# Optimization experiments

Hardware: AMD Instinct MI355X
Metric: run time of the kernel (lower is better)

Reference implementation:

```python
import jax, jax.numpy as jnp
import numpy as np
import math

NUM_HEADS = 8
EPS = 1e-5
LEAKY_SLOPE = 0.01


def _attention(q, k, v, mask):
    # q:[S,64] k,v:[T,64] -> [S,64]; scale by sqrt(d) per source (q.shape[1])
    s = (q @ k.T) / math.sqrt(q.shape[1])
    if mask:
        S, T = s.shape
        tri = jnp.tril(jnp.ones((S, T), dtype=bool))
        s = jnp.where(tri, s, -jnp.inf)
    return jax.nn.softmax(s, axis=1) @ v


def _mha(q, k, v, w_o, mask):
    # all heads share the same (q,k,v) in the source, so cat over heads == tile
    head = _attention(q, k, v, mask)            # [S,64]
    concat = jnp.tile(head, (1, NUM_HEADS))     # [S,512]
    return concat @ w_o


def _layernorm(x, g, b):
    mu = jnp.mean(x, axis=-1, keepdims=True)
    var = jnp.var(x, axis=-1, keepdims=True)
    return (x - mu) * jax.lax.rsqrt(var + EPS) * g + b


def setup_inputs() -> dict:
    key = jax.random.key(0)
    ks = jax.random.split(key, 12)
    S, D, P, H = 8192, 512, 64, 2048
    sd = 1.0 / math.sqrt(D)
    return {
        "encoder_output": jax.random.normal(ks[0], (S, D), jnp.float32),
        "previous_stage_output": jax.random.normal(ks[1], (S, D), jnp.float32),
        "wq_m": jax.random.normal(ks[2], (D, P), jnp.float32) * sd,
        "wk_m": jax.random.normal(ks[3], (D, P), jnp.float32) * sd,
        "wv_m": jax.random.normal(ks[4], (D, P), jnp.float32) * sd,
        "wq_c": jax.random.normal(ks[5], (D, P), jnp.float32) * sd,
        "wk_c": jax.random.normal(ks[6], (D, P), jnp.float32) * sd,
        "wv_c": jax.random.normal(ks[7], (D, P), jnp.float32) * sd,
        "w_o": jax.random.normal(ks[8], (D, D), jnp.float32) * sd,
        "ln_g": jnp.ones((D,), jnp.float32),
        "ln_b": jnp.zeros((D,), jnp.float32),
        "w1": jax.random.normal(ks[9], (D, H), jnp.float32) * sd,
        "b1": jnp.zeros((H,), jnp.float32),
        "w2": jax.random.normal(ks[10], (H, D), jnp.float32) * (1.0 / math.sqrt(H)),
        "b2": jnp.zeros((D,), jnp.float32),
    }


def reference(encoder_output, previous_stage_output, wq_m, wk_m, wv_m,
              wq_c, wk_c, wv_c, w_o, ln_g, ln_b, w1, b1, w2, b2):
    prev = previous_stage_output
    # masked (causal) self-attention over previous decoder output
    masked_mh = _mha(prev @ wq_m, prev @ wk_m, prev @ wv_m, w_o, mask=True)
    # cross attention: q from masked output, k/v from encoder output
    mh = _mha(masked_mh @ wq_c, encoder_output @ wk_c, encoder_output @ wv_c,
              w_o, mask=False)
    x = _layernorm(mh + prev, ln_g, ln_b)
    h = x @ w1 + b1
    h = jnp.where(h >= 0, h, LEAKY_SLOPE * h)
    ffn = h @ w2 + b2
    out = _layernorm(ffn + x, ln_g, ln_b)
    return (encoder_output, out)
```

## Files before the change

kernel.cpp:

```cpp
#include <hip/hip_runtime.h>
#include <hip/hip_bf16.h>

typedef unsigned short u16;
typedef __attribute__((ext_vector_type(4))) float f32x4;
typedef __attribute__((ext_vector_type(8))) __bf16 bf16x8;
typedef __attribute__((ext_vector_type(8))) short short8;
typedef __attribute__((ext_vector_type(4))) short s16x4;

constexpr int SEQ = 8192;
constexpr int DM  = 512;
constexpr int HD  = 64;
constexpr int HFF = 2048;

__device__ __forceinline__ float b2f(u16 u){
  union { unsigned int i; float f; } v; v.i = ((unsigned int)u) << 16; return v.f;
}
__device__ __forceinline__ u16 f2b(float f){
  union { float f; unsigned int i; } v; v.f = f;
  unsigned int r = v.i + 0x7FFFu + ((v.i >> 16) & 1u);
  return (u16)(r >> 16);
}

__device__ __forceinline__ void gload16(const u16* g, u16* lds){
  __builtin_amdgcn_global_load_lds(
      (const __attribute__((address_space(1))) void*)g,
      (__attribute__((address_space(3))) void*)lds, 16, 0, 0);
}

__global__ __launch_bounds__(256) void copycvt_k(const float* __restrict__ in,
                                                 float* __restrict__ outf,
                                                 u16* __restrict__ outb, long n8){
  long i = blockIdx.x * 256L + threadIdx.x;
  if(i >= n8) return;
  f32x4 a = ((const f32x4*)in)[i*2];
  f32x4 b = ((const f32x4*)in)[i*2+1];
  ((f32x4*)outf)[i*2]   = a;
  ((f32x4*)outf)[i*2+1] = b;
  u16 ov[8];
  for(int j=0;j<4;j++){ ov[j] = f2b(a[j]); ov[4+j] = f2b(b[j]); }
  ((short8*)outb)[i] = *(short8*)ov;
}

__global__ __launch_bounds__(256) void cvt_k(const float* __restrict__ in,
                                             u16* __restrict__ out, long n8){
  long i = blockIdx.x * 256L + threadIdx.x;
  if(i >= n8) return;
  f32x4 a = ((const f32x4*)in)[i*2];
  f32x4 b = ((const f32x4*)in)[i*2+1];
  u16 ov[8];
  for(int j=0;j<4;j++){ ov[j] = f2b(a[j]); ov[4+j] = f2b(b[j]); }
  ((short8*)out)[i] = *(short8*)ov;
}

__global__ __launch_bounds__(256) void wtrans6_k(const float* __restrict__ w0,
                                                 const float* __restrict__ w1,
                                                 const float* __restrict__ w2,
                                                 const float* __restrict__ w3,
                                                 const float* __restrict__ w4,
                                                 const float* __restrict__ w5,
                                                 u16* __restrict__ out){
  __shared__ u16 t[32][33];
  const float* ins[6] = {w0,w1,w2,w3,w4,w5};
  const float* in = ins[blockIdx.z];
  u16* o = out + (long)blockIdx.z * 32768;
  int c0 = blockIdx.x*32, r0 = blockIdx.y*32;
  int tx = threadIdx.x, ty = threadIdx.y;
  for(int i=0;i<4;i++)
    t[ty+i*8][tx] = f2b(in[(long)(r0+ty+i*8)*HD + c0+tx]);
  __syncthreads();
  for(int i=0;i<4;i++) o[(long)(c0+ty+i*8)*DM + r0+tx] = t[tx][ty+i*8];
}

template<int IN_F>
__global__ __launch_bounds__(256) void transpose_k(const void* __restrict__ inp,
                                                   u16* __restrict__ out, int R, int C){
  __shared__ u16 t[32][33];
  int c0 = blockIdx.x*32, r0 = blockIdx.y*32;
  int tx = threadIdx.x, ty = threadIdx.y;
  for(int i=0;i<4;i++){
    long idx = (long)(r0+ty+i*8)*C + c0+tx;
    u16 v;
    if constexpr (IN_F) v = f2b(((const float*)inp)[idx]);
    else                v = ((const u16*)inp)[idx];
    t[ty+i*8][tx] = v;
  }
  __syncthreads();
  for(int i=0;i<4;i++) out[(long)(c0+ty+i*8)*R + r0+tx] = t[tx][ty+i*8];
}

__global__ __launch_bounds__(256) void vtrans2_k(const u16* __restrict__ v0,
                                                 u16* __restrict__ o0,
                                                 const u16* __restrict__ v1,
                                                 u16* __restrict__ o1){
  __shared__ u16 t[32][33];
  const u16* in = blockIdx.z ? v1 : v0;
  u16* o = blockIdx.z ? o1 : o0;
  int c0 = blockIdx.x*32, r0 = blockIdx.y*32;
  int tx = threadIdx.x, ty = threadIdx.y;
  for(int i=0;i<4;i++) t[ty+i*8][tx] = in[(long)(r0+ty+i*8)*HD + c0+tx];
  __syncthreads();
  for(int i=0;i<4;i++) o[(long)(c0+ty+i*8)*SEQ + r0+tx] = t[tx][ty+i*8];
}

__global__ __launch_bounds__(256) void wosum_k(const float* __restrict__ wo,
                                               u16* __restrict__ outT){
  int tid = blockIdx.x*256 + threadIdx.x;
  int n = tid >> 6, p = tid & 63;
  float s = 0.f;
  for(int h=0; h<8; h++) s += wo[(long)(h*64+p)*DM + n];
  outT[n*64+p] = f2b(s);
}

template<bool WRITE_BF>
__global__ __launch_bounds__(256) void add_ln(const u16* __restrict__ Xa,
                                              const float* __restrict__ Xb,
                                              const float* __restrict__ G,
                                              const float* __restrict__ Bb,
                                              float* __restrict__ OutF,
                                              u16* __restrict__ OutB){
  int row  = blockIdx.x*4 + (threadIdx.x>>6);
  int lane = threadIdx.x & 63;
  short8 a8 = *(const short8*)&Xa[(long)row*DM + lane*8];
  f32x4 b0 = *(const f32x4*)&Xb[(long)row*DM + lane*8];
  f32x4 b1 = *(const f32x4*)&Xb[(long)row*DM + lane*8 + 4];
  float x[8]; float s=0.f, s2=0.f;
  for(int i=0;i<8;i++){
    float bv = (i<4) ? b0[i] : b1[i-4];
    x[i] = b2f((u16)a8[i]) + bv;
    s += x[i]; s2 += x[i]*x[i];
  }
  for(int o=1;o<64;o<<=1){ s += __shfl_xor(s,o); s2 += __shfl_xor(s2,o); }
  float mu  = s * (1.f/DM);
  float var = s2 * (1.f/DM) - mu*mu;
  float rstd = rsqrtf(var + 1e-5f);
  f32x4 g0 = *(const f32x4*)&G[lane*8];
  f32x4 g1 = *(const f32x4*)&G[lane*8+4];
  f32x4 p0 = *(const f32x4*)&Bb[lane*8];
  f32x4 p1 = *(const f32x4*)&Bb[lane*8+4];
  float of[8]; u16 ob[8];
  for(int i=0;i<8;i++){
    float gv = (i<4)?g0[i]:g1[i-4], bv2 = (i<4)?p0[i]:p1[i-4];
    float v = (x[i]-mu)*rstd*gv + bv2;
    of[i] = v; ob[i] = f2b(v);
  }
  *(f32x4*)&OutF[(long)row*DM + lane*8]     = *(f32x4*)&of[0];
  *(f32x4*)&OutF[(long)row*DM + lane*8 + 4] = *(f32x4*)&of[4];
  if constexpr (WRITE_BF)
    *(short8*)&OutB[(long)row*DM + lane*8] = *(short8*)ob;
}

template<int BM,int BN,int EPI,bool DBUF>
__global__ __launch_bounds__(256) void gemm2(const u16* __restrict__ A,
                                             const u16* __restrict__ Bt,
                                             u16* __restrict__ C,
                                             const float* __restrict__ bias,
                                             int N, int K, long sB, long sC){
  constexpr int WR=2, WC=2;
  constexpr int WM = BM/WR, WN = BN/WC;
  constexpr int MF = WM/16, NF = WN/16;
  constexpr int NB = DBUF ? 2 : 1;
  __shared__ u16 As[NB][BM*64];
  __shared__ u16 Bs[NB][BN*64];

  const int tid = threadIdx.x;
  const int wid = tid >> 6, lane = tid & 63;
  const int g = lane >> 4, lr = lane & 15;
  const int m0 = blockIdx.x * BM;
  const int n0 = blockIdx.y * BN;
  Bt += (long)blockIdx.z * sB;
  C  += (long)blockIdx.z * sC;
  const int wr = wid / WC, wc = wid % WC;

  f32x4 acc[MF][NF];
  for(int m=0;m<MF;m++) for(int n=0;n<NF;n++) acc[m][n] = (f32x4)0.f;

  auto stage = [&](const u16* src, int base_row, u16* lds, int rows, int k0){
    const int cpw = rows/32;
    for(int i=0;i<cpw;i++){
      int chunk = wid*cpw + i;
      int Lb = chunk*1024;
      int L  = Lb + lane*16;
      int row = L >> 7, cb = L & 127;
      int scb = cb ^ ((row&7)<<4);
      gload16(&src[(long)(base_row+row)*K + k0 + (scb>>1)], lds + (Lb>>1));
    }
  };
  auto compute = [&](const u16* As_, const u16* Bs_){
    for(int kc=0;kc<2;kc++){
      const int co = (kc*32 + g*8) ^ ((lr&7)<<3);
      bf16x8 af[MF], bfr[NF];
      for(int m=0;m<MF;m++) af[m]  = *(const bf16x8*)&As_[(wr*WM+m*16+lr)*64 + co];
      for(int n=0;n<NF;n++) bfr[n] = *(const bf16x8*)&Bs_[(wc*WN+n*16+lr)*64 + co];
      for(int m=0;m<MF;m++)
        for(int n=0;n<NF;n++)
          acc[m][n] = __builtin_amdgcn_mfma_f32_16x16x32_bf16(af[m], bfr[n], acc[m][n], 0,0,0);
    }
  };

  const int nk = K/64;
  if constexpr (DBUF){
    stage(A, m0, As[0], BM, 0);
    stage(Bt, n0, Bs[0], BN, 0);
    __syncthreads();
    int cur = 0;
    for(int t=0;t<nk;t++){
      if(t+1<nk){
        stage(A, m0, As[cur^1], BM, (t+1)*64);
        stage(Bt, n0, Bs[cur^1], BN, (t+1)*64);
      }
      compute(As[cur], Bs[cur]);
      __syncthreads();
      cur ^= 1;
    }
  } else {
    for(int t=0;t<nk;t++){
      stage(A, m0, As[0], BM, t*64);
      stage(Bt, n0, Bs[0], BN, t*64);
      __syncthreads();
      compute(As[0], Bs[0]);
      __syncthreads();
    }
  }
  for(int m=0;m<MF;m++){
    int row = m0 + wr*WM + m*16 + g*4;
    for(int n=0;n<NF;n++){
      int col = n0 + wc*WN + n*16 + lr;
      float bv = 0.f;
      if constexpr (EPI>=1) bv = bias[col];
      for(int j=0;j<4;j++){
        float v = acc[m][n][j] + bv;
        if constexpr (EPI==2) v = (v >= 0.f) ? v : 0.01f*v;
        C[(long)(row+j)*N + col] = f2b(v);
      }
    }
  }
}

template<bool CAUSAL>
__global__ __launch_bounds__(256) void attn_part_k(const u16* __restrict__ Q,
                                                   const u16* __restrict__ Km,
                                                   const u16* __restrict__ Vt,
                                                   u16* __restrict__ Op,
                                                   float* __restrict__ Ml){
  constexpr int LDK = 72;
  constexpr int NCH = 16;
  constexpr int CTI = 8;
  __shared__ u16 Ks[64*LDK];
  __shared__ u16 Vs[64*LDK];
  __shared__ u16 Ps[4*16*LDK];

  const int qb = blockIdx.x, ci = blockIdx.y;
  if(CAUSAL && ci*CTI > qb) return;

  const int tid = threadIdx.x, wid = tid>>6, lane = tid&63;
  const int g = lane>>4, lr = lane&15, r4 = g*4;
  const int qrow = qb*64 + wid*16;

  bf16x8 qf[2];
  for(int kc=0;kc<2;kc++){
    bf16x8 t = *(const bf16x8*)&Q[(long)(qrow + lr)*HD + kc*32 + g*8];
    for(int i=0;i<8;i++) t[i] = (__bf16)((float)t[i] * 0.1803368801f);
    qf[kc] = t;
  }

  f32x4 o[4]; for(int n=0;n<4;n++) o[n] = (f32x4)0.f;
  float mst = -1e30f, lst = 0.f;

  const int tdiag = qb - ci*CTI;
  const int tmax = CAUSAL ? min(CTI, tdiag + 1) : CTI;

  const int sr0 = tid>>3, sc0 = (tid&7)*8;
  short8 rK0, rK1, rV0, rV1;
  {
    const int kv0 = ci*512;
    rK0 = *(const short8*)&Km[(long)(kv0+sr0)*HD + sc0];
    rK1 = *(const short8*)&Km[(long)(kv0+sr0+32)*HD + sc0];
    rV0 = *(const short8*)&Vt[(long)sr0*SEQ + kv0 + sc0];
    rV1 = *(const short8*)&Vt[(long)(sr0+32)*SEQ + kv0 + sc0];
  }

  for(int t=0; t<tmax; ++t){
    const int kv0 = ci*512 + t*64;
    __syncthreads();
    *(short8*)&Ks[sr0*LDK + sc0]      = rK0;
    *(short8*)&Ks[(sr0+32)*LDK + sc0] = rK1;
    *(short8*)&Vs[sr0*LDK + sc0]      = rV0;
    *(short8*)&Vs[(sr0+32)*LDK + sc0] = rV1;
    __syncthreads();
    if(t+1 < tmax){
      const int kn = kv0 + 64;
      rK0 = *(const short8*)&Km[(long)(kn+sr0)*HD + sc0];
      rK1 = *(const short8*)&Km[(long)(kn+sr0+32)*HD + sc0];
      rV0 = *(const short8*)&Vt[(long)sr0*SEQ + kn + sc0];
      rV1 = *(const short8*)&Vt[(long)(sr0+32)*SEQ + kn + sc0];
    }

    f32x4 s[4]; for(int n=0;n<4;n++) s[n] = (f32x4)0.f;
    for(int kc=0;kc<2;kc++){
      for(int n=0;n<4;n++){
        bf16x8 kf = *(const bf16x8*)&Ks[(n*16+lr)*LDK + kc*32 + g*8];
        s[n] = __builtin_amdgcn_mfma_f32_16x16x32_bf16(kf, qf[kc], s[n], 0,0,0);
      }
    }
    if(CAUSAL && t == tdiag){
      int row = qrow + lr;
      for(int n=0;n<4;n++)
        for(int j=0;j<4;j++)
          if(kv0 + n*16 + r4 + j > row) s[n][j] = -1e30f;
    }
    float m01 = fmaxf(fmaxf(s[0][0],s[0][1]), fmaxf(s[0][2],s[0][3]));
    float m11 = fmaxf(fmaxf(s[1][0],s[1][1]), fmaxf(s[1][2],s[1][3]));
    float m21 = fmaxf(fmaxf(s[2][0],s[2][1]), fmaxf(s[2][2],s[2][3]));
    float m31 = fmaxf(fmaxf(s[3][0],s[3][1]), fmaxf(s[3][2],s[3][3]));
    float pmax = fmaxf(fmaxf(m01,m11), fmaxf(m21,m31));
    pmax = fmaxf(pmax, __shfl_xor(pmax,16));
    pmax = fmaxf(pmax, __shfl_xor(pmax,32));
    if(__any(pmax > mst + 8.f)){
      float mn = fmaxf(mst, pmax);
      float fac = exp2f(mst - mn);
      mst = mn; lst *= fac;
      float fj0 = __shfl(fac, r4+0), fj1 = __shfl(fac, r4+1);
      float fj2 = __shfl(fac, r4+2), fj3 = __shfl(fac, r4+3);
      for(int n=0;n<4;n++){
        o[n][0] *= fj0; o[n][1] *= fj1; o[n][2] *= fj2; o[n][3] *= fj3;
      }
    }
    float rs = 0.f;
    for(int n=0;n<4;n++){
      u16 w[4];
      for(int j=0;j<4;j++){
        float p = exp2f(s[n][j] - mst);
        rs += p;
        __bf16 pb = (__bf16)p;
        union { __bf16 b; u16 u; } cv; cv.b = pb;
        w[j] = cv.u;
      }
      *(s16x4*)&Ps[(wid*16 + lr)*LDK + n*16 + r4] = *(s16x4*)w;
    }
    rs += __shfl_xor(rs,16); rs += __shfl_xor(rs,32);
    lst += rs;
    for(int kc=0;kc<2;kc++){
      bf16x8 pf = *(const bf16x8*)&Ps[(wid*16 + lr)*LDK + kc*32 + g*8];
      for(int n=0;n<4;n++){
        bf16x8 vf = *(const bf16x8*)&Vs[(n*16+lr)*LDK + kc*32 + g*8];
        o[n] = __builtin_amdgcn_mfma_f32_16x16x32_bf16(pf, vf, o[n], 0,0,0);
      }
    }
  }
  const long pr = (long)(qb*NCH + ci)*64;
  for(int n=0;n<4;n++)
    for(int j=0;j<4;j++)
      Op[(pr + wid*16 + r4 + j)*64 + n*16 + lr] = f2b(o[n][j]);
  if(lane < 16){
    Ml[(pr + wid*16 + lr)*2]     = mst;
    Ml[(pr + wid*16 + lr)*2 + 1] = lst;
  }
}

template<bool CAUSAL>
__global__ __launch_bounds__(256) void attn_red_k(const u16* __restrict__ Op,
                                                  const float* __restrict__ Ml,
                                                  u16* __restrict__ O){
  int r = blockIdx.x*4 + (threadIdx.x>>6);
  int d = threadIdx.x & 63;
  int qb = r >> 6, rt = r & 63;
  int nch = CAUSAL ? (qb>>3) + 1 : 16;
  long base = (long)qb*16*64 + rt;
  float m = -1e30f;
  for(int i=0;i<nch;i++) m = fmaxf(m, Ml[(base + i*64)*2]);
  float L = 0.f, acc = 0.f;
  for(int i=0;i<nch;i++){
    float mi = Ml[(base + i*64)*2], li = Ml[(base + i*64)*2 + 1];
    float w = exp2f(mi - m);
    L   += li * w;
    acc += w * b2f(Op[(base + i*64)*64 + d]);
  }
  O[(long)r*HD + d] = f2b(acc / L);
}

extern "C" void kernel_launch(void* const* d_in, const int* in_sizes, int n_in,
                              void* d_out, int out_size, void* d_ws, size_t ws_size,
                              hipStream_t stream){
  const float* enc  = (const float*)d_in[0];
  const float* prev = (const float*)d_in[1];
  const float* wq_m = (const float*)d_in[2];
  const float* wk_m = (const float*)d_in[3];
  const float* wv_m = (const float*)d_in[4];
  const float* wq_c = (const float*)d_in[5];
  const float* wk_c = (const float*)d_in[6];
  const float* wv_c = (const float*)d_in[7];
  const float* w_o  = (const float*)d_in[8];
  const float* ln_g = (const float*)d_in[9];
  const float* ln_b = (const float*)d_in[10];
  const float* w1   = (const float*)d_in[11];
  const float* b1   = (const float*)d_in[12];
  const float* w2   = (const float*)d_in[13];
  const float* b2   = (const float*)d_in[14];
  float* out = (float*)d_out;
  u16* ws  = (u16*)d_ws;

  u16* wq_m_t = ws;
  u16* wk_c_t = wq_m_t + 4*32768;
  u16* wost   = wq_m_t + 6*32768;
  u16* w1_t   = wost   + 32768;
  u16* w2_t   = w1_t   + 1048576;
  u16* enc_b  = w2_t   + 1048576;
  u16* prev_b = enc_b  + 4194304;
  u16* q_m    = prev_b + 4194304;
  u16* k_m    = q_m    + 524288;
  u16* v_m    = k_m    + 524288;
  u16* v_m_t  = v_m    + 524288;
  u16* head_m = v_m_t  + 524288;
  u16* k_c    = head_m + 524288;
  u16* v_c    = k_c    + 524288;
  u16* v_c_t  = v_c    + 524288;
  u16* q_c    = v_c_t  + 524288;
  u16* head_c = q_c    + 524288;
  u16* mmh    = head_c + 524288;
  u16* mh     = mmh    + 4194304;
  u16* xb     = mh     + 4194304;
  float* xf   = (float*)(xb + 4194304);
  u16* hbuf   = enc_b;
  u16* ffn    = mh;
  u16* Op     = mmh;
  float* Ml   = (float*)(Op + (long)128*16*64*64);

  dim3 b256(256), tb(32,8);

  copycvt_k<<<dim3(2048), b256, 0, stream>>>(enc, out, enc_b, (long)SEQ*DM/8);
  cvt_k<<<dim3(2048), b256, 0, stream>>>(prev, prev_b, (long)SEQ*DM/8);

  wtrans6_k<<<dim3(2,16,6), tb, 0, stream>>>(wq_m, wk_m, wv_m, wq_c, wk_c, wv_c, wq_m_t);
  transpose_k<1><<<dim3(64,16), tb, 0, stream>>>(w1, w1_t, DM, HFF);
  transpose_k<1><<<dim3(16,64), tb, 0, stream>>>(w2, w2_t, HFF, DM);
  wosum_k<<<dim3(128), b256, 0, stream>>>(w_o, wost);

  gemm2<64,64,0,true><<<dim3(SEQ/64,1,3), b256, 0, stream>>>(prev_b, wq_m_t, q_m, nullptr, HD, DM, 32768, 524288);
  gemm2<64,64,0,true><<<dim3(SEQ/64,1,2), b256, 0, stream>>>(enc_b,  wk_c_t, k_c, nullptr, HD, DM, 32768, 524288);
  vtrans2_k<<<dim3(2,256,2), tb, 0, stream>>>(v_m, v_m_t, v_c, v_c_t);

  attn_part_k<true><<<dim3(SEQ/64, 16), b256, 0, stream>>>(q_m, k_m, v_m_t, Op, Ml);
  attn_red_k<true><<<dim3(SEQ/4), b256, 0, stream>>>(Op, Ml, head_m);
  gemm2<64,128,0,false><<<dim3(SEQ/64,4,1), b256, 0, stream>>>(head_m, wost, mmh, nullptr, DM, HD, 0, 0);

  gemm2<64,64,0,false><<<dim3(SEQ/64,1,1), b256, 0, stream>>>(mmh, wq_m_t + 3*32768, q_c, nullptr, HD, DM, 0, 0);
  attn_part_k<false><<<dim3(SEQ/64, 16), b256, 0, stream>>>(q_c, k_c, v_c_t, Op, Ml);
  attn_red_k<false><<<dim3(SEQ/4), b256, 0, stream>>>(Op, Ml, head_c);
  gemm2<64,128,0,false><<<dim3(SEQ/64,4,1), b256, 0, stream>>>(head_c, wost, mh, nullptr, DM, HD, 0, 0);

  add_ln<true><<<dim3(SEQ/4), b256, 0, stream>>>(mh, prev, ln_g, ln_b, xf, xb);

  gemm2<128,128,2,false><<<dim3(SEQ/128,HFF/128,1), b256, 0, stream>>>(xb, w1_t, hbuf, b1, HFF, DM, 0, 0);
  gemm2<64,128,1,false><<<dim3(SEQ/64,4,1),         b256, 0, stream>>>(hbuf, w2_t, ffn, b2, DM, HFF, 0, 0);

  add_ln<false><<<dim3(SEQ/4), b256, 0, stream>>>(ffn, xf, ln_g, ln_b, out + (long)SEQ*DM, nullptr);
}
```

Measured before the change: 225.0 us.

## Swizzle attention LDS tiles, raise MFMA wave priority, merge input conversion kernels

Replaces the padded LDS layout for the K, V and P tiles in the attention kernel with an unpadded 64-wide layout that XOR-swizzles 8-element column groups by row, so fragment reads avoid bank conflicts and use less shared memory. Wraps the MFMA loops in s_setprio so waves issuing matrix work get scheduling priority. Merges the two fp32-to-bf16 conversion kernels into one launch with a 2D grid, saving one kernel launch. The swizzle must match on the write and read sides; any indexing mismatch would corrupt the results.

New measurement: 222.0 us. Within noise of the previous version (-1.3%).

```diff
diff --git a/kernel.cpp b/kernel.cpp
--- a/kernel.cpp
+++ b/kernel.cpp
@@ -27,29 +27,24 @@
       (__attribute__((address_space(3))) void*)lds, 16, 0, 0);
 }
 
-__global__ __launch_bounds__(256) void copycvt_k(const float* __restrict__ in,
-                                                 float* __restrict__ outf,
-                                                 u16* __restrict__ outb, long n8){
+__global__ __launch_bounds__(256) void cvt2_k(const float* __restrict__ enc,
+                                              const float* __restrict__ prev,
+                                              float* __restrict__ outf,
+                                              u16* __restrict__ enc_b,
+                                              u16* __restrict__ prev_b, long n8){
   long i = blockIdx.x * 256L + threadIdx.x;
   if(i >= n8) return;
+  const float* in = blockIdx.y ? prev : enc;
+  u16* ob = blockIdx.y ? prev_b : enc_b;
   f32x4 a = ((const f32x4*)in)[i*2];
   f32x4 b = ((const f32x4*)in)[i*2+1];
-  ((f32x4*)outf)[i*2]   = a;
-  ((f32x4*)outf)[i*2+1] = b;
+  if(!blockIdx.y){
+    ((f32x4*)outf)[i*2]   = a;
+    ((f32x4*)outf)[i*2+1] = b;
+  }
   u16 ov[8];
   for(int j=0;j<4;j++){ ov[j] = f2b(a[j]); ov[4+j] = f2b(b[j]); }
-  ((short8*)outb)[i] = *(short8*)ov;
-}
-
-__global__ __launch_bounds__(256) void cvt_k(const float* __restrict__ in,
-                                             u16* __restrict__ out, long n8){
-  long i = blockIdx.x * 256L + threadIdx.x;
-  if(i >= n8) return;
-  f32x4 a = ((const f32x4*)in)[i*2];
-  f32x4 b = ((const f32x4*)in)[i*2+1];
-  u16 ov[8];
-  for(int j=0;j<4;j++){ ov[j] = f2b(a[j]); ov[4+j] = f2b(b[j]); }
-  ((short8*)out)[i] = *(short8*)ov;
+  ((short8*)ob)[i] = *(short8*)ov;
 }
 
 __global__ __launch_bounds__(256) void wtrans6_k(const float* __restrict__ w0,
@@ -242,12 +237,11 @@
                                                    const u16* __restrict__ Vt,
                                                    u16* __restrict__ Op,
                                                    float* __restrict__ Ml){
-  constexpr int LDK = 72;
   constexpr int NCH = 16;
   constexpr int CTI = 8;
-  __shared__ u16 Ks[64*LDK];
-  __shared__ u16 Vs[64*LDK];
-  __shared__ u16 Ps[4*16*LDK];
+  __shared__ u16 Ks[64*64];
+  __shared__ u16 Vs[64*64];
+  __shared__ u16 Ps[4*16*64];
 
   const int qb = blockIdx.x, ci = blockIdx.y;
   if(CAUSAL && ci*CTI > qb) return;
@@ -255,6 +249,7 @@
   const int tid = threadIdx.x, wid = tid>>6, lane = tid&63;
   const int g = lane>>4, lr = lane&15, r4 = g*4;
   const int qrow = qb*64 + wid*16;
+  const int rsw = (lr&7)<<3;
 
   bf16x8 qf[2];
   for(int kc=0;kc<2;kc++){
@@ -270,6 +265,7 @@
   const int tmax = CAUSAL ? min(CTI, tdiag + 1) : CTI;
 
   const int sr0 = tid>>3, sc0 = (tid&7)*8;
+  const int wsw = (sr0&7)<<3;
   short8 rK0, rK1, rV0, rV1;
   {
     const int kv0 = ci*512;
@@ -282,10 +278,10 @@
   for(int t=0; t<tmax; ++t){
     const int kv0 = ci*512 + t*64;
     __syncthreads();
-    *(short8*)&Ks[sr0*LDK + sc0]      = rK0;
-    *(short8*)&Ks[(sr0+32)*LDK + sc0] = rK1;
-    *(short8*)&Vs[sr0*LDK + sc0]      = rV0;
-    *(short8*)&Vs[(sr0+32)*LDK + sc0] = rV1;
+    *(short8*)&Ks[sr0*64      + (sc0 ^ wsw)] = rK0;
+    *(short8*)&Ks[(sr0+32)*64 + (sc0 ^ wsw)] = rK1;
+    *(short8*)&Vs[sr0*64      + (sc0 ^ wsw)] = rV0;
+    *(short8*)&Vs[(sr0+32)*64 + (sc0 ^ wsw)] = rV1;
     __syncthreads();
     if(t+1 < tmax){
       const int kn = kv0 + 64;
@@ -296,12 +292,15 @@
     }
 
     f32x4 s[4]; for(int n=0;n<4;n++) s[n] = (f32x4)0.f;
+    __builtin_amdgcn_s_setprio(1);
     for(int kc=0;kc<2;kc++){
+      const int co = (kc*32 + g*8) ^ rsw;
       for(int n=0;n<4;n++){
-        bf16x8 kf = *(const bf16x8*)&Ks[(n*16+lr)*LDK + kc*32 + g*8];
+        bf16x8 kf = *(const bf16x8*)&Ks[(n*16+lr)*64 + co];
         s[n] = __builtin_amdgcn_mfma_f32_16x16x32_bf16(kf, qf[kc], s[n], 0,0,0);
       }
     }
+    __builtin_amdgcn_s_setprio(0);
     if(CAUSAL && t == tdiag){
       int row = qrow + lr;
       for(int n=0;n<4;n++)
@@ -335,17 +334,20 @@
         union { __bf16 b; u16 u; } cv; cv.b = pb;
         w[j] = cv.u;
       }
-      *(s16x4*)&Ps[(wid*16 + lr)*LDK + n*16 + r4] = *(s16x4*)w;
+      *(s16x4*)&Ps[(wid*16 + lr)*64 + ((n*16 + r4) ^ rsw)] = *(s16x4*)w;
     }
     rs += __shfl_xor(rs,16); rs += __shfl_xor(rs,32);
     lst += rs;
+    __builtin_amdgcn_s_setprio(1);
     for(int kc=0;kc<2;kc++){
-      bf16x8 pf = *(const bf16x8*)&Ps[(wid*16 + lr)*LDK + kc*32 + g*8];
+      const int co = (kc*32 + g*8) ^ rsw;
+      bf16x8 pf = *(const bf16x8*)&Ps[(wid*16 + lr)*64 + co];
       for(int n=0;n<4;n++){
-        bf16x8 vf = *(const bf16x8*)&Vs[(n*16+lr)*LDK + kc*32 + g*8];
+        bf16x8 vf = *(const bf16x8*)&Vs[(n*16+lr)*64 + co];
         o[n] = __builtin_amdgcn_mfma_f32_16x16x32_bf16(pf, vf, o[n], 0,0,0);
       }
     }
+    __builtin_amdgcn_s_setprio(0);
   }
   const long pr = (long)(qb*NCH + ci)*64;
   for(int n=0;n<4;n++)
@@ -427,8 +429,7 @@
 
   dim3 b256(256), tb(32,8);
 
-  copycvt_k<<<dim3(2048), b256, 0, stream>>>(enc, out, enc_b, (long)SEQ*DM/8);
-  cvt_k<<<dim3(2048), b256, 0, stream>>>(prev, prev_b, (long)SEQ*DM/8);
+  cvt2_k<<<dim3(2048,2), b256, 0, stream>>>(enc, prev, out, enc_b, prev_b, (long)SEQ*DM/8);
 
   wtrans6_k<<<dim3(2,16,6), tb, 0, stream>>>(wq_m, wk_m, wv_m, wq_c, wk_c, wv_c, wq_m_t);
   transpose_k<1><<<dim3(64,16), tb, 0, stream>>>(w1, w1_t, DM, HFF);
```
